# Kernel optimization log

Hardware: AMD Instinct MI355X
Metric: run time of the kernel (lower is better)

Reference implementation:

```python
import jax, jax.numpy as jnp
import numpy as np

N_NODES = 50000
N_EDGES = 800000
D = 64
N_BASIS = 8


def setup_inputs() -> dict:
    key = jax.random.key(0)
    ks = jax.random.split(key, 16)
    inp = {
        "p": jax.random.normal(ks[0], (N_NODES, D), dtype=jnp.float32),
        "idx_i": jax.random.randint(ks[1], (N_EDGES,), 0, N_NODES),
        "idx_j": jax.random.randint(ks[2], (N_EDGES,), 0, N_NODES),
        "basis": jax.random.normal(ks[3], (N_EDGES, N_BASIS), dtype=jnp.float32),
        # pp_layer MLP: [64, 64, 64], activation tanh between layers
        "pp_W1": jax.random.normal(ks[4], (D, D), dtype=jnp.float32) / np.sqrt(D),
        "pp_b1": jnp.zeros((D,), dtype=jnp.float32),
        "pp_W2": jax.random.normal(ks[5], (D, D), dtype=jnp.float32) / np.sqrt(D),
        "pp_b2": jnp.zeros((D,), dtype=jnp.float32),
        # pi_layer MLP: n_neurons = [128, 64, 64, 64*8], activation=None, last layer no bias
        "pi_W1": jax.random.normal(ks[6], (2 * D, D), dtype=jnp.float32) / np.sqrt(2 * D),
        "pi_b1": jnp.zeros((D,), dtype=jnp.float32),
        "pi_W2": jax.random.normal(ks[7], (D, D), dtype=jnp.float32) / np.sqrt(D),
        "pi_b2": jnp.zeros((D,), dtype=jnp.float32),
        "pi_W3": jax.random.normal(ks[8], (D, D * N_BASIS), dtype=jnp.float32) / np.sqrt(D),
        # ii_layer MLP: [64, 64, 64], activation tanh between layers
        "ii_W1": jax.random.normal(ks[9], (D, D), dtype=jnp.float32) / np.sqrt(D),
        "ii_b1": jnp.zeros((D,), dtype=jnp.float32),
        "ii_W2": jax.random.normal(ks[10], (D, D), dtype=jnp.float32) / np.sqrt(D),
        "ii_b2": jnp.zeros((D,), dtype=jnp.float32),
    }
    return inp


def reference(p, idx_i, idx_j, basis,
              pp_W1, pp_b1, pp_W2, pp_b2,
              pi_W1, pi_b1, pi_W2, pi_b2, pi_W3,
              ii_W1, ii_b1, ii_W2, ii_b2):
    # pp_layer: node MLP (tanh between layers, no activation after last)
    p1 = jnp.tanh(p @ pp_W1 + pp_b1) @ pp_W2 + pp_b2          # [N, D]

    # PILayer: gather endpoint features, concat, linear MLP (activation=None), basis contraction
    inter = jnp.concatenate([p1[idx_i], p1[idx_j]], axis=-1)  # [E, 2D]
    inter = inter @ pi_W1 + pi_b1                              # [E, D]
    inter = inter @ pi_W2 + pi_b2                              # [E, D]
    inter = inter @ pi_W3                                      # [E, D*n_basis] (no bias)
    inter = inter.reshape(inter.shape[0], D, N_BASIS)          # [E, D, n_basis]
    i1 = jnp.einsum('ecb,eb->ec', inter, basis)                # [E, D]

    # ii_layer: edge MLP
    i1 = jnp.tanh(i1 @ ii_W1 + ii_b1) @ ii_W2 + ii_b2          # [E, D]

    # IPLayer: scatter_add edge features back to nodes (dim_size = p1.shape[0])
    out = jax.ops.segment_sum(i1, idx_j, num_segments=p1.shape[0])  # [N, D]
    return out
```

## Files before the change

### kernel.cpp

```cpp
#include <hip/hip_runtime.h>

#define N_NODES 50000
#define N_EDGES 800000
#define NPAD 50176

typedef float f32x4 __attribute__((ext_vector_type(4)));
typedef short bf16x8 __attribute__((ext_vector_type(8)));

__device__ __forceinline__ float fast_tanh(float x) {
  float e = __expf(2.0f * x);
  float r;
  asm("v_rcp_f32 %0, %1" : "=v"(r) : "v"(e + 1.0f));
  return fmaf(-2.0f, r, 1.0f);
}

__device__ __forceinline__ unsigned short f2bf_rne(float x) {
  unsigned u = __float_as_uint(x);
  unsigned r = u + 0x7FFFu + ((u >> 16) & 1u);
  return (unsigned short)(r >> 16);
}

__global__ __launch_bounds__(256) void prep_all_kernel(
    const float* __restrict__ piW1, const float* __restrict__ pib1,
    const float* __restrict__ piW2, const float* __restrict__ pib2,
    const float* __restrict__ piW3, const float* __restrict__ iiW1,
    const float* __restrict__ iiW2,
    float* __restrict__ W12, float* __restrict__ b12,
    unsigned short* __restrict__ Bpack, unsigned short* __restrict__ W2pack) {
  int gid = blockIdx.x * 256 + threadIdx.x;
  if (gid < 32768) {
    int j = gid & 7;
    int lane = (gid >> 3) & 63;
    int ct = (gid >> 9) & 3;
    int ks = gid >> 11;
    int kidx = ks * 32 + ((lane >> 4) << 3) + j;
    int col = ct * 16 + (lane & 15);
    int k = kidx >> 3, b = kidx & 7;
    float acc = 0.f;
    #pragma unroll 8
    for (int mm = 0; mm < 64; ++mm)
      acc = fmaf(piW3[k * 512 + mm * 8 + b], iiW1[mm * 64 + col], acc);
    Bpack[gid] = f2bf_rne(acc);
  } else if (gid < 41024) {
    int g1 = gid - 32768;
    if (g1 < 8192) {
      int m = g1 >> 6, c = g1 & 63;
      float acc = 0.f;
      #pragma unroll 8
      for (int k = 0; k < 64; ++k) acc = fmaf(piW1[m * 64 + k], piW2[k * 64 + c], acc);
      W12[g1] = acc;
    } else {
      int c = g1 - 8192;
      float acc = pib2[c];
      for (int k = 0; k < 64; ++k) acc = fmaf(pib1[k], piW2[k * 64 + c], acc);
      b12[c] = acc;
    }
  } else if (gid < 45120) {
    int g2 = gid - 41024;
    int j = g2 & 7;
    int lane = (g2 >> 3) & 63;
    int ct = (g2 >> 9) & 3;
    int ks = g2 >> 11;
    int kidx = ks * 32 + ((lane >> 4) << 3) + j;
    int col = ct * 16 + (lane & 15);
    W2pack[g2] = f2bf_rne(iiW2[kidx * 64 + col]);
  }
}

__global__ __launch_bounds__(256) void hist_kernel(
    const int* __restrict__ idx_j, int* __restrict__ counts) {
  int e = blockIdx.x * 256 + threadIdx.x;
  if (e < N_EDGES) atomicAdd(&counts[idx_j[e]], 1);
}

__global__ __launch_bounds__(1024) void scanA_kernel(
    const int* __restrict__ counts, int* __restrict__ cursors,
    int* __restrict__ blocksums) {
  __shared__ int buf[1024];
  int b = blockIdx.x, tid = threadIdx.x;
  int idx = b * 1024 + tid;
  int v = counts[idx];
  buf[tid] = v;
  __syncthreads();
  for (int off = 1; off < 1024; off <<= 1) {
    int t = (tid >= off) ? buf[tid - off] : 0;
    __syncthreads();
    buf[tid] += t;
    __syncthreads();
  }
  cursors[idx] = buf[tid] - v;
  if (tid == 1023) blocksums[b] = buf[1023];
}

__global__ __launch_bounds__(1024) void scanC_kernel(
    int* __restrict__ cursors, const int* __restrict__ blocksums) {
  __shared__ int sb[49];
  __shared__ int sbase;
  int b = blockIdx.x, tid = threadIdx.x;
  if (tid < 49) sb[tid] = blocksums[tid];
  __syncthreads();
  if (tid == 0) {
    int acc = 0;
    for (int i = 0; i < b; ++i) acc += sb[i];
    sbase = acc;
  }
  __syncthreads();
  cursors[b * 1024 + tid] += sbase;
}

__global__ __launch_bounds__(256) void sort_scatter_kernel(
    const int* __restrict__ idx_i, const int* __restrict__ idx_j,
    int* __restrict__ cursors,
    int2* __restrict__ sorted_ij, int* __restrict__ sorted_e) {
  int e = blockIdx.x * 256 + threadIdx.x;
  if (e < N_EDGES) {
    int j = idx_j[e];
    int pos = atomicAdd(&cursors[j], 1);
    sorted_ij[pos] = make_int2(idx_i[e], j);
    sorted_e[pos] = e;
  }
}

__global__ __launch_bounds__(256) void node_kernel(
    const float* __restrict__ p,
    const float* __restrict__ ppW1, const float* __restrict__ ppb1,
    const float* __restrict__ ppW2, const float* __restrict__ ppb2,
    const float* __restrict__ W12,
    float* __restrict__ qa, float* __restrict__ qb) {
  __shared__ float sW1[64 * 64];
  __shared__ float sW2[64 * 64];
  __shared__ float sW12[128 * 64];
  __shared__ float sb1[64], sb2[64];
  __shared__ float sX[4][8][64];
  int tid = threadIdx.x;
  for (int i = tid; i < 64 * 64; i += 256) { sW1[i] = ppW1[i]; sW2[i] = ppW2[i]; }
  for (int i = tid; i < 128 * 64; i += 256) sW12[i] = W12[i];
  if (tid < 64) { sb1[tid] = ppb1[tid]; sb2[tid] = ppb2[tid]; }
  __syncthreads();
  int wave = tid >> 6, lane = tid & 63;
  int rowbase = blockIdx.x * 32 + wave * 8;

  float4* sXf4 = (float4*)&sX[wave][0][0];
  for (int t = lane; t < 128; t += 64) {
    int r = t >> 4, c4 = t & 15;
    int row = rowbase + r;
    float4 v = make_float4(0.f, 0.f, 0.f, 0.f);
    if (row < N_NODES) v = ((const float4*)p)[row * 16 + c4];
    sXf4[t] = v;
  }
  __syncthreads();

  float h[8];
  #pragma unroll
  for (int r = 0; r < 8; ++r) h[r] = sb1[lane];
  for (int k = 0; k < 64; ++k) {
    float w = sW1[k * 64 + lane];
    #pragma unroll
    for (int r = 0; r < 8; ++r) h[r] = fmaf(sX[wave][r][k], w, h[r]);
  }
  #pragma unroll
  for (int r = 0; r < 8; ++r) h[r] = fast_tanh(h[r]);
  __syncthreads();
  #pragma unroll
  for (int r = 0; r < 8; ++r) sX[wave][r][lane] = h[r];
  __syncthreads();

  float g[8];
  #pragma unroll
  for (int r = 0; r < 8; ++r) g[r] = sb2[lane];
  for (int k = 0; k < 64; ++k) {
    float w = sW2[k * 64 + lane];
    #pragma unroll
    for (int r = 0; r < 8; ++r) g[r] = fmaf(sX[wave][r][k], w, g[r]);
  }
  __syncthreads();
  #pragma unroll
  for (int r = 0; r < 8; ++r) sX[wave][r][lane] = g[r];
  __syncthreads();

  float a[8], b[8];
  #pragma unroll
  for (int r = 0; r < 8; ++r) { a[r] = 0.f; b[r] = 0.f; }
  for (int k = 0; k < 64; ++k) {
    float wa = sW12[k * 64 + lane];
    float wb = sW12[(64 + k) * 64 + lane];
    #pragma unroll
    for (int r = 0; r < 8; ++r) {
      float x = sX[wave][r][k];
      a[r] = fmaf(x, wa, a[r]);
      b[r] = fmaf(x, wb, b[r]);
    }
  }
  #pragma unroll
  for (int r = 0; r < 8; ++r) {
    int row = rowbase + r;
    if (row < N_NODES) {
      qa[row * 64 + lane] = a[r];
      qb[row * 64 + lane] = b[r];
    }
  }
}

__global__ __launch_bounds__(1024, 8) void edge_kernel(
    const int2* __restrict__ sorted_ij, const int* __restrict__ sorted_e,
    const float* __restrict__ basis,
    const float* __restrict__ qa, const float* __restrict__ qb,
    const float* __restrict__ b12,
    const unsigned short* __restrict__ Bpack,
    const unsigned short* __restrict__ W2pack,
    const float* __restrict__ iib1, const float* __restrict__ iib2,
    float* __restrict__ out) {
  __shared__ __align__(16) unsigned short sB[32768];
  float* sH2 = (float*)sB;
  unsigned short* sT = sB;
  float* sF = (float*)sB;

  int tid = threadIdx.x;
  int e0 = blockIdx.x * 256;

  for (int t = tid; t < 4096; t += 1024) {
    int e = t >> 4, q = t & 15;
    int2 se = sorted_ij[e0 + e];
    float4 va = ((const float4*)qa)[se.x * 16 + q];
    float4 vb = ((const float4*)qb)[se.y * 16 + q];
    float4 vc = ((const float4*)b12)[q];
    float4 h;
    h.x = va.x + vb.x + vc.x;
    h.y = va.y + vb.y + vc.y;
    h.z = va.z + vb.z + vc.z;
    h.w = va.w + vb.w + vc.w;
    int dw = e * 64 + ((q * 4) ^ ((e & 7) << 3));
    *((float4*)(sH2 + dw)) = h;
  }
  __syncthreads();

  int w = tid >> 6, l = tid & 63;
  int m = l & 15, s = l >> 4;
  int eloc = w * 16 + m;
  int swz = (eloc & 7) << 3;

  float h2r[16];
  #pragma unroll
  for (int t = 0; t < 16; ++t) h2r[t] = sH2[eloc * 64 + ((t * 4 + s) ^ swz)];

  float bas[8];
  {
    int eorig = sorted_e[e0 + eloc];
    const float4* bp = (const float4*)(basis + (size_t)eorig * 8);
    float4 b0 = bp[0], b1 = bp[1];
    bas[0] = b0.x; bas[1] = b0.y; bas[2] = b0.z; bas[3] = b0.w;
    bas[4] = b1.x; bas[5] = b1.y; bas[6] = b1.z; bas[7] = b1.w;
  }
  __syncthreads();

  {
    const uint4* g = (const uint4*)Bpack;
    uint4* d = (uint4*)sB;
    #pragma unroll
    for (int t = 0; t < 4; ++t) d[tid + t * 1024] = g[tid + t * 1024];
  }
  __syncthreads();

  f32x4 c0, c1, c2, c3;
  {
    float v0 = iib1[m], v1 = iib1[16 + m], v2 = iib1[32 + m], v3 = iib1[48 + m];
    c0 = (f32x4){v0, v0, v0, v0};
    c1 = (f32x4){v1, v1, v1, v1};
    c2 = (f32x4){v2, v2, v2, v2};
    c3 = (f32x4){v3, v3, v3, v3};
  }

  const bf16x8* Bl = (const bf16x8*)sB;
  #pragma unroll
  for (int ks = 0; ks < 16; ++ks) {
    bf16x8 B0 = Bl[(ks * 4 + 0) * 64 + l];
    bf16x8 B1 = Bl[(ks * 4 + 1) * 64 + l];
    bf16x8 B2 = Bl[(ks * 4 + 2) * 64 + l];
    bf16x8 B3 = Bl[(ks * 4 + 3) * 64 + l];
    float hv = h2r[ks];
    union { unsigned u[4]; bf16x8 v; } A;
    #pragma unroll
    for (int j = 0; j < 4; ++j) {
      float p0 = hv * bas[2 * j];
      float p1 = hv * bas[2 * j + 1];
      asm("v_cvt_pk_bf16_f32 %0, %1, %2" : "=v"(A.u[j]) : "v"(p0), "v"(p1));
    }
    c0 = __builtin_amdgcn_mfma_f32_16x16x32_bf16(A.v, B0, c0, 0, 0, 0);
    c1 = __builtin_amdgcn_mfma_f32_16x16x32_bf16(A.v, B1, c1, 0, 0, 0);
    c2 = __builtin_amdgcn_mfma_f32_16x16x32_bf16(A.v, B2, c2, 0, 0, 0);
    c3 = __builtin_amdgcn_mfma_f32_16x16x32_bf16(A.v, B3, c3, 0, 0, 0);
  }
  __syncthreads();

  #pragma unroll
  for (int r = 0; r < 4; ++r) {
    int row = w * 16 + s * 4 + r;
    sT[row * 72 + 0 * 16 + m] = f2bf_rne(fast_tanh(c0[r]));
    sT[row * 72 + 1 * 16 + m] = f2bf_rne(fast_tanh(c1[r]));
    sT[row * 72 + 2 * 16 + m] = f2bf_rne(fast_tanh(c2[r]));
    sT[row * 72 + 3 * 16 + m] = f2bf_rne(fast_tanh(c3[r]));
  }
  __syncthreads();

  f32x4 d0, d1, d2, d3;
  {
    float v0 = iib2[m], v1 = iib2[16 + m], v2 = iib2[32 + m], v3 = iib2[48 + m];
    d0 = (f32x4){v0, v0, v0, v0};
    d1 = (f32x4){v1, v1, v1, v1};
    d2 = (f32x4){v2, v2, v2, v2};
    d3 = (f32x4){v3, v3, v3, v3};
  }
  const bf16x8* Wl = (const bf16x8*)W2pack;
  #pragma unroll
  for (int ks = 0; ks < 2; ++ks) {
    bf16x8 Af = *(const bf16x8*)(sT + eloc * 72 + ks * 32 + s * 8);
    d0 = __builtin_amdgcn_mfma_f32_16x16x32_bf16(Af, Wl[(ks * 4 + 0) * 64 + l], d0, 0, 0, 0);
    d1 = __builtin_amdgcn_mfma_f32_16x16x32_bf16(Af, Wl[(ks * 4 + 1) * 64 + l], d1, 0, 0, 0);
    d2 = __builtin_amdgcn_mfma_f32_16x16x32_bf16(Af, Wl[(ks * 4 + 2) * 64 + l], d2, 0, 0, 0);
    d3 = __builtin_amdgcn_mfma_f32_16x16x32_bf16(Af, Wl[(ks * 4 + 3) * 64 + l], d3, 0, 0, 0);
  }

  #pragma unroll
  for (int h = 0; h < 2; ++h) {
    __syncthreads();
    if ((w >> 3) == h) {
      int wl = w & 7;
      #pragma unroll
      for (int r = 0; r < 4; ++r) {
        int row = wl * 16 + s * 4 + r;
        sF[row * 68 + 0  + m] = d0[r];
        sF[row * 68 + 16 + m] = d1[r];
        sF[row * 68 + 32 + m] = d2[r];
        sF[row * 68 + 48 + m] = d3[r];
      }
    }
    __syncthreads();
    {
      int base_e = e0 + h * 128 + w * 8;
      float acc = sF[(w * 8) * 68 + l];
      int cur_j = sorted_ij[base_e].y;
      #pragma unroll
      for (int rr = 1; rr < 8; ++rr) {
        int nj = sorted_ij[base_e + rr].y;
        float v = sF[(w * 8 + rr) * 68 + l];
        if (nj == cur_j) {
          acc += v;
        } else {
          atomicAdd(&out[(size_t)cur_j * 64 + l], acc);
          acc = v;
          cur_j = nj;
        }
      }
      atomicAdd(&out[(size_t)cur_j * 64 + l], acc);
    }
  }
}

extern "C" void kernel_launch(void* const* d_in, const int* in_sizes, int n_in,
                              void* d_out, int out_size, void* d_ws, size_t ws_size,
                              hipStream_t stream) {
  const float* p     = (const float*)d_in[0];
  const int*   idx_i = (const int*)d_in[1];
  const int*   idx_j = (const int*)d_in[2];
  const float* basis = (const float*)d_in[3];
  const float* ppW1  = (const float*)d_in[4];
  const float* ppb1  = (const float*)d_in[5];
  const float* ppW2  = (const float*)d_in[6];
  const float* ppb2  = (const float*)d_in[7];
  const float* piW1  = (const float*)d_in[8];
  const float* pib1  = (const float*)d_in[9];
  const float* piW2  = (const float*)d_in[10];
  const float* pib2  = (const float*)d_in[11];
  const float* piW3  = (const float*)d_in[12];
  const float* iiW1  = (const float*)d_in[13];
  const float* iib1  = (const float*)d_in[14];
  const float* iiW2  = (const float*)d_in[15];
  const float* iib2  = (const float*)d_in[16];

  float* ws  = (float*)d_ws;
  float* qa  = ws;
  float* qb  = ws + 3200000;
  float* W12 = ws + 6400000;
  float* b12 = ws + 6408192;
  unsigned short* Bpack  = (unsigned short*)(ws + 6408256);
  unsigned short* W2pack = (unsigned short*)(ws + 6424640);
  int* counts    = (int*)(ws + 6426688);
  int* cursors   = (int*)(ws + 6476864);
  int* blocksums = (int*)(ws + 6527040);
  int2* sorted_ij = (int2*)(ws + 6527104);
  int* sorted_e   = (int*)(ws + 8127104);

  hipMemsetAsync(d_out, 0, (size_t)out_size * sizeof(float), stream);
  hipMemsetAsync(counts, 0, (size_t)NPAD * sizeof(int), stream);
  prep_all_kernel<<<177, 256, 0, stream>>>(piW1, pib1, piW2, pib2, piW3, iiW1, iiW2,
                                           W12, b12, Bpack, W2pack);
  hist_kernel<<<3125, 256, 0, stream>>>(idx_j, counts);
  scanA_kernel<<<49, 1024, 0, stream>>>(counts, cursors, blocksums);
  scanC_kernel<<<49, 1024, 0, stream>>>(cursors, blocksums);
  sort_scatter_kernel<<<3125, 256, 0, stream>>>(idx_i, idx_j, cursors,
                                                sorted_ij, sorted_e);
  node_kernel<<<1563, 256, 0, stream>>>(p, ppW1, ppb1, ppW2, ppb2, W12, qa, qb);
  edge_kernel<<<3125, 1024, 0, stream>>>(sorted_ij, sorted_e, basis,
                                         qa, qb, b12, Bpack, W2pack,
                                         iib1, iib2, (float*)d_out);
}
```

Baseline: 303.1 us.

## Fuse prep, histogram and node MLP into one front kernel; single-pass scan

Merges weight prep, the idx_j histogram and the node MLP into one launch that uses block-index ranges for the different roles. The node path now computes piW1 then piW2 in sequence instead of a precomputed W12, and reloads a single 16KB shared weight buffer per layer with float4 LDS reads. The two-kernel scan becomes one kernel in which each block redundantly sums all preceding counts. This removes several launches and the serial dependency between prep and node work, at the cost of more FLOPs per node, extra barriers, and redundant global reads in the scan.

Measured after the change: 300.6 us. Within noise of the previous version (-0.8%).

```diff
diff --git a/kernel.cpp b/kernel.cpp
--- a/kernel.cpp
+++ b/kernel.cpp
@@ -20,67 +20,167 @@
   return (unsigned short)(r >> 16);
 }
 
-__global__ __launch_bounds__(256) void prep_all_kernel(
+__device__ __forceinline__ void gemm8(const float* __restrict__ sXrow,
+                                      const float* __restrict__ sW,
+                                      int lane, float acc[8]) {
+  for (int k = 0; k < 64; k += 4) {
+    float w0 = sW[k * 64 + lane];
+    float w1 = sW[(k + 1) * 64 + lane];
+    float w2 = sW[(k + 2) * 64 + lane];
+    float w3 = sW[(k + 3) * 64 + lane];
+    #pragma unroll
+    for (int r = 0; r < 8; ++r) {
+      float4 x = *(const float4*)(sXrow + r * 64 + k);
+      acc[r] = fmaf(x.x, w0, fmaf(x.y, w1, fmaf(x.z, w2, fmaf(x.w, w3, acc[r]))));
+    }
+  }
+}
+
+__global__ __launch_bounds__(256) void front_kernel(
+    const float* __restrict__ p, const int* __restrict__ idx_j,
+    const float* __restrict__ ppW1, const float* __restrict__ ppb1,
+    const float* __restrict__ ppW2, const float* __restrict__ ppb2,
     const float* __restrict__ piW1, const float* __restrict__ pib1,
     const float* __restrict__ piW2, const float* __restrict__ pib2,
     const float* __restrict__ piW3, const float* __restrict__ iiW1,
     const float* __restrict__ iiW2,
-    float* __restrict__ W12, float* __restrict__ b12,
+    int* __restrict__ counts,
+    float* __restrict__ qa, float* __restrict__ qb, float* __restrict__ b12,
     unsigned short* __restrict__ Bpack, unsigned short* __restrict__ W2pack) {
-  int gid = blockIdx.x * 256 + threadIdx.x;
-  if (gid < 32768) {
-    int j = gid & 7;
-    int lane = (gid >> 3) & 63;
-    int ct = (gid >> 9) & 3;
-    int ks = gid >> 11;
-    int kidx = ks * 32 + ((lane >> 4) << 3) + j;
-    int col = ct * 16 + (lane & 15);
-    int k = kidx >> 3, b = kidx & 7;
-    float acc = 0.f;
-    #pragma unroll 8
-    for (int mm = 0; mm < 64; ++mm)
-      acc = fmaf(piW3[k * 512 + mm * 8 + b], iiW1[mm * 64 + col], acc);
-    Bpack[gid] = f2bf_rne(acc);
-  } else if (gid < 41024) {
-    int g1 = gid - 32768;
-    if (g1 < 8192) {
-      int m = g1 >> 6, c = g1 & 63;
+  int bid = blockIdx.x;
+  int tid = threadIdx.x;
+
+  if (bid >= 1708) {
+    int e = (bid - 1708) * 256 + tid;
+    if (e < N_EDGES) atomicAdd(&counts[idx_j[e]], 1);
+    return;
+  }
+  if (bid >= 1563) {
+    int gid = (bid - 1563) * 256 + tid;
+    if (gid < 32768) {
+      int j = gid & 7;
+      int lane = (gid >> 3) & 63;
+      int ct = (gid >> 9) & 3;
+      int ks = gid >> 11;
+      int kidx = ks * 32 + ((lane >> 4) << 3) + j;
+      int col = ct * 16 + (lane & 15);
+      int k = kidx >> 3, b = kidx & 7;
       float acc = 0.f;
       #pragma unroll 8
-      for (int k = 0; k < 64; ++k) acc = fmaf(piW1[m * 64 + k], piW2[k * 64 + c], acc);
-      W12[g1] = acc;
-    } else {
-      int c = g1 - 8192;
+      for (int mm = 0; mm < 64; ++mm)
+        acc = fmaf(piW3[k * 512 + mm * 8 + b], iiW1[mm * 64 + col], acc);
+      Bpack[gid] = f2bf_rne(acc);
+    } else if (gid < 32832) {
+      int c = gid - 32768;
       float acc = pib2[c];
       for (int k = 0; k < 64; ++k) acc = fmaf(pib1[k], piW2[k * 64 + c], acc);
       b12[c] = acc;
-    }
-  } else if (gid < 45120) {
-    int g2 = gid - 41024;
-    int j = g2 & 7;
-    int lane = (g2 >> 3) & 63;
-    int ct = (g2 >> 9) & 3;
-    int ks = g2 >> 11;
-    int kidx = ks * 32 + ((lane >> 4) << 3) + j;
-    int col = ct * 16 + (lane & 15);
-    W2pack[g2] = f2bf_rne(iiW2[kidx * 64 + col]);
-  }
-}
-
-__global__ __launch_bounds__(256) void hist_kernel(
-    const int* __restrict__ idx_j, int* __restrict__ counts) {
-  int e = blockIdx.x * 256 + threadIdx.x;
-  if (e < N_EDGES) atomicAdd(&counts[idx_j[e]], 1);
-}
-
-__global__ __launch_bounds__(1024) void scanA_kernel(
-    const int* __restrict__ counts, int* __restrict__ cursors,
-    int* __restrict__ blocksums) {
+    } else if (gid < 36928) {
+      int g2 = gid - 32832;
+      int j = g2 & 7;
+      int lane = (g2 >> 3) & 63;
+      int ct = (g2 >> 9) & 3;
+      int ks = g2 >> 11;
+      int kidx = ks * 32 + ((lane >> 4) << 3) + j;
+      int col = ct * 16 + (lane & 15);
+      W2pack[g2] = f2bf_rne(iiW2[kidx * 64 + col]);
+    }
+    return;
+  }
+
+  __shared__ float sW[64 * 64];
+  __shared__ float sX[4][8][64];
+  __shared__ float sY[4][8][64];
+  int wave = tid >> 6, lane = tid & 63;
+  int rowbase = bid * 32 + wave * 8;
+
+  float4* sXf4 = (float4*)&sX[wave][0][0];
+  for (int t = lane; t < 128; t += 64) {
+    int r = t >> 4, c4 = t & 15;
+    int row = rowbase + r;
+    float4 v = make_float4(0.f, 0.f, 0.f, 0.f);
+    if (row < N_NODES) v = ((const float4*)p)[row * 16 + c4];
+    sXf4[t] = v;
+  }
+  for (int i = tid; i < 4096; i += 256) sW[i] = ppW1[i];
+  __syncthreads();
+  float h[8];
+  {
+    float bv = ppb1[lane];
+    #pragma unroll
+    for (int r = 0; r < 8; ++r) h[r] = bv;
+  }
+  gemm8(&sX[wave][0][0], sW, lane, h);
+  #pragma unroll
+  for (int r = 0; r < 8; ++r) sY[wave][r][lane] = fast_tanh(h[r]);
+  __syncthreads();
+  for (int i = tid; i < 4096; i += 256) sW[i] = ppW2[i];
+  __syncthreads();
+  float g[8];
+  {
+    float bv = ppb2[lane];
+    #pragma unroll
+    for (int r = 0; r < 8; ++r) g[r] = bv;
+  }
+  gemm8(&sY[wave][0][0], sW, lane, g);
+  #pragma unroll
+  for (int r = 0; r < 8; ++r) sX[wave][r][lane] = g[r];
+  __syncthreads();
+  for (int i = tid; i < 4096; i += 256) sW[i] = piW1[i];
+  __syncthreads();
+  float t1[8] = {0, 0, 0, 0, 0, 0, 0, 0};
+  gemm8(&sX[wave][0][0], sW, lane, t1);
+  #pragma unroll
+  for (int r = 0; r < 8; ++r) sY[wave][r][lane] = t1[r];
+  __syncthreads();
+  for (int i = tid; i < 4096; i += 256) sW[i] = piW1[4096 + i];
+  __syncthreads();
+  float t2[8] = {0, 0, 0, 0, 0, 0, 0, 0};
+  gemm8(&sX[wave][0][0], sW, lane, t2);
+  __syncthreads();
+  #pragma unroll
+  for (int r = 0; r < 8; ++r) sX[wave][r][lane] = t2[r];
+  __syncthreads();
+  for (int i = tid; i < 4096; i += 256) sW[i] = piW2[i];
+  __syncthreads();
+  float a[8] = {0, 0, 0, 0, 0, 0, 0, 0};
+  float b[8] = {0, 0, 0, 0, 0, 0, 0, 0};
+  for (int k = 0; k < 64; k += 4) {
+    float w0 = sW[k * 64 + lane];
+    float w1 = sW[(k + 1) * 64 + lane];
+    float w2 = sW[(k + 2) * 64 + lane];
+    float w3 = sW[(k + 3) * 64 + lane];
+    #pragma unroll
+    for (int r = 0; r < 8; ++r) {
+      float4 x = *(const float4*)(&sY[wave][r][k]);
+      float4 y = *(const float4*)(&sX[wave][r][k]);
+      a[r] = fmaf(x.x, w0, fmaf(x.y, w1, fmaf(x.z, w2, fmaf(x.w, w3, a[r]))));
+      b[r] = fmaf(y.x, w0, fmaf(y.y, w1, fmaf(y.z, w2, fmaf(y.w, w3, b[r]))));
+    }
+  }
+  #pragma unroll
+  for (int r = 0; r < 8; ++r) {
+    int row = rowbase + r;
+    if (row < N_NODES) {
+      qa[row * 64 + lane] = a[r];
+      qb[row * 64 + lane] = b[r];
+    }
+  }
+}
+
+__global__ __launch_bounds__(1024) void scan_kernel(
+    const int* __restrict__ counts, int* __restrict__ cursors) {
   __shared__ int buf[1024];
+  __shared__ int red[16];
   int b = blockIdx.x, tid = threadIdx.x;
   int idx = b * 1024 + tid;
   int v = counts[idx];
   buf[tid] = v;
+  int partial = 0;
+  for (int i = tid; i < b * 1024; i += 1024) partial += counts[i];
+  #pragma unroll
+  for (int off = 32; off >= 1; off >>= 1) partial += __shfl_down(partial, off, 64);
+  if ((tid & 63) == 0) red[tid >> 6] = partial;
   __syncthreads();
   for (int off = 1; off < 1024; off <<= 1) {
     int t = (tid >= off) ? buf[tid - off] : 0;
@@ -88,24 +188,10 @@
     buf[tid] += t;
     __syncthreads();
   }
-  cursors[idx] = buf[tid] - v;
-  if (tid == 1023) blocksums[b] = buf[1023];
-}
-
-__global__ __launch_bounds__(1024) void scanC_kernel(
-    int* __restrict__ cursors, const int* __restrict__ blocksums) {
-  __shared__ int sb[49];
-  __shared__ int sbase;
-  int b = blockIdx.x, tid = threadIdx.x;
-  if (tid < 49) sb[tid] = blocksums[tid];
-  __syncthreads();
-  if (tid == 0) {
-    int acc = 0;
-    for (int i = 0; i < b; ++i) acc += sb[i];
-    sbase = acc;
-  }
-  __syncthreads();
-  cursors[b * 1024 + tid] += sbase;
+  int base = 0;
+  #pragma unroll
+  for (int i = 0; i < 16; ++i) base += red[i];
+  cursors[idx] = base + buf[tid] - v;
 }
 
 __global__ __launch_bounds__(256) void sort_scatter_kernel(
@@ -118,86 +204,6 @@
     int pos = atomicAdd(&cursors[j], 1);
     sorted_ij[pos] = make_int2(idx_i[e], j);
     sorted_e[pos] = e;
-  }
-}
-
-__global__ __launch_bounds__(256) void node_kernel(
-    const float* __restrict__ p,
-    const float* __restrict__ ppW1, const float* __restrict__ ppb1,
-    const float* __restrict__ ppW2, const float* __restrict__ ppb2,
-    const float* __restrict__ W12,
-    float* __restrict__ qa, float* __restrict__ qb) {
-  __shared__ float sW1[64 * 64];
-  __shared__ float sW2[64 * 64];
-  __shared__ float sW12[128 * 64];
-  __shared__ float sb1[64], sb2[64];
-  __shared__ float sX[4][8][64];
-  int tid = threadIdx.x;
-  for (int i = tid; i < 64 * 64; i += 256) { sW1[i] = ppW1[i]; sW2[i] = ppW2[i]; }
-  for (int i = tid; i < 128 * 64; i += 256) sW12[i] = W12[i];
-  if (tid < 64) { sb1[tid] = ppb1[tid]; sb2[tid] = ppb2[tid]; }
-  __syncthreads();
-  int wave = tid >> 6, lane = tid & 63;
-  int rowbase = blockIdx.x * 32 + wave * 8;
-
-  float4* sXf4 = (float4*)&sX[wave][0][0];
-  for (int t = lane; t < 128; t += 64) {
-    int r = t >> 4, c4 = t & 15;
-    int row = rowbase + r;
-    float4 v = make_float4(0.f, 0.f, 0.f, 0.f);
-    if (row < N_NODES) v = ((const float4*)p)[row * 16 + c4];
-    sXf4[t] = v;
-  }
-  __syncthreads();
-
-  float h[8];
-  #pragma unroll
-  for (int r = 0; r < 8; ++r) h[r] = sb1[lane];
-  for (int k = 0; k < 64; ++k) {
-    float w = sW1[k * 64 + lane];
-    #pragma unroll
-    for (int r = 0; r < 8; ++r) h[r] = fmaf(sX[wave][r][k], w, h[r]);
-  }
-  #pragma unroll
-  for (int r = 0; r < 8; ++r) h[r] = fast_tanh(h[r]);
-  __syncthreads();
-  #pragma unroll
-  for (int r = 0; r < 8; ++r) sX[wave][r][lane] = h[r];
-  __syncthreads();
-
-  float g[8];
-  #pragma unroll
-  for (int r = 0; r < 8; ++r) g[r] = sb2[lane];
-  for (int k = 0; k < 64; ++k) {
-    float w = sW2[k * 64 + lane];
-    #pragma unroll
-    for (int r = 0; r < 8; ++r) g[r] = fmaf(sX[wave][r][k], w, g[r]);
-  }
-  __syncthreads();
-  #pragma unroll
-  for (int r = 0; r < 8; ++r) sX[wave][r][lane] = g[r];
-  __syncthreads();
-
-  float a[8], b[8];
-  #pragma unroll
-  for (int r = 0; r < 8; ++r) { a[r] = 0.f; b[r] = 0.f; }
-  for (int k = 0; k < 64; ++k) {
-    float wa = sW12[k * 64 + lane];
-    float wb = sW12[(64 + k) * 64 + lane];
-    #pragma unroll
-    for (int r = 0; r < 8; ++r) {
-      float x = sX[wave][r][k];
-      a[r] = fmaf(x, wa, a[r]);
-      b[r] = fmaf(x, wb, b[r]);
-    }
-  }
-  #pragma unroll
-  for (int r = 0; r < 8; ++r) {
-    int row = rowbase + r;
-    if (row < N_NODES) {
-      qa[row * 64 + lane] = a[r];
-      qb[row * 64 + lane] = b[r];
-    }
   }
 }
 
@@ -380,26 +386,22 @@
   float* ws  = (float*)d_ws;
   float* qa  = ws;
   float* qb  = ws + 3200000;
-  float* W12 = ws + 6400000;
-  float* b12 = ws + 6408192;
-  unsigned short* Bpack  = (unsigned short*)(ws + 6408256);
-  unsigned short* W2pack = (unsigned short*)(ws + 6424640);
-  int* counts    = (int*)(ws + 6426688);
-  int* cursors   = (int*)(ws + 6476864);
-  int* blocksums = (int*)(ws + 6527040);
-  int2* sorted_ij = (int2*)(ws + 6527104);
-  int* sorted_e   = (int*)(ws + 8127104);
+  float* b12 = ws + 6400000;
+  unsigned short* Bpack  = (unsigned short*)(ws + 6400064);
+  unsigned short* W2pack = (unsigned short*)(ws + 6416448);
+  int* counts    = (int*)(ws + 6418496);
+  int* cursors   = (int*)(ws + 6468672);
+  int2* sorted_ij = (int2*)(ws + 6518848);
+  int* sorted_e   = (int*)(ws + 8118848);
 
   hipMemsetAsync(d_out, 0, (size_t)out_size * sizeof(float), stream);
   hipMemsetAsync(counts, 0, (size_t)NPAD * sizeof(int), stream);
-  prep_all_kernel<<<177, 256, 0, stream>>>(piW1, pib1, piW2, pib2, piW3, iiW1, iiW2,
-                                           W12, b12, Bpack, W2pack);
-  hist_kernel<<<3125, 256, 0, stream>>>(idx_j, counts);
-  scanA_kernel<<<49, 1024, 0, stream>>>(counts, cursors, blocksums);
-  scanC_kernel<<<49, 1024, 0, stream>>>(cursors, blocksums);
+  front_kernel<<<4833, 256, 0, stream>>>(p, idx_j, ppW1, ppb1, ppW2, ppb2,
+                                         piW1, pib1, piW2, pib2, piW3, iiW1, iiW2,
+                                         counts, qa, qb, b12, Bpack, W2pack);
+  scan_kernel<<<49, 1024, 0, stream>>>(counts, cursors);
   sort_scatter_kernel<<<3125, 256, 0, stream>>>(idx_i, idx_j, cursors,
                                                 sorted_ij, sorted_e);
-  node_kernel<<<1563, 256, 0, stream>>>(p, ppW1, ppb1, ppW2, ppb2, W12, qa, qb);
   edge_kernel<<<3125, 1024, 0, stream>>>(sorted_ij, sorted_e, basis,
                                          qa, qb, b12, Bpack, W2pack,
                                          iib1, iib2, (float*)d_out);
```
